# Performance work log

Measured on AMD Instinct MI355X. Metric: run time of the kernel, lower is better.

The kernel has to match this reference:

```python
import jax, jax.numpy as jnp
import numpy as np

ALPHA = 0.2  # LeakyReLU negative slope


def setup_inputs() -> dict:
    key = jax.random.key(0)
    k1, k2, k3, k4 = jax.random.split(key, 4)
    bs, n, fin = 8, 1024, 256
    heads, fo = 8, 64
    h = jax.random.normal(k1, (bs, n, fin), dtype=jnp.float32)
    adj = jax.random.randint(k2, (bs, n, n), 0, 2, dtype=jnp.int32)
    # W stored as [in_features, heads*out] so Wh = h @ W (same math as torch Linear)
    W = jax.random.normal(k3, (fin, heads * fo), dtype=jnp.float32) * 0.1
    a = jax.random.normal(k4, (heads, 2 * fo), dtype=jnp.float32) * 0.1
    return {"h": h, "adj": adj, "W": W, "a": a}


def reference(h, adj, W, a):
    bs, n, _ = h.shape
    heads, two_fo = a.shape
    fo = two_fo // 2
    # Wh: [bs, n, heads, fo]
    Wh = (h @ W).reshape(bs, n, heads, fo)
    a_src, a_dst = a[:, :fo], a[:, fo:]
    # Additive attention decomposed: e[b,h,i,j] = leaky_relu(src[b,h,i] + dst[b,h,j])
    e_src = jnp.einsum('bnhf,hf->bhn', Wh, a_src)  # [bs, heads, n]
    e_dst = jnp.einsum('bnhf,hf->bhn', Wh, a_dst)
    e = e_src[:, :, :, None] + e_dst[:, :, None, :]  # [bs, heads, n, n]
    e = jnp.where(e > 0, e, ALPHA * e)  # LeakyReLU
    e = jnp.where(adj[:, None, :, :] == 0, -jnp.inf, e)
    attn = jax.nn.softmax(e, axis=-1)  # [bs, heads, n, n]
    # h_prime[b,i,h,f] = sum_j attn[b,h,i,j] * Wh[b,j,h,f]
    h_prime = jnp.einsum('bhij,bjhf->bihf', attn, Wh)
    return h_prime.reshape(bs, n, heads * fo)
```

## Files before the change

kernel.cpp:

```cpp
#include <hip/hip_runtime.h>
#include <hip/hip_bf16.h>
#include <math.h>

#define BS 8
#define NN 1024
#define FIN 256
#define HEADS 8
#define FO 64
#define NH (HEADS*FO)
static constexpr float ALPHA = 0.2f;
static constexpr float LOG2E = 1.4426950408889634f;

typedef short bf16x8 __attribute__((ext_vector_type(8)));
typedef float f32x4  __attribute__((ext_vector_type(4)));
typedef unsigned short u16;
typedef unsigned u32;
typedef u16 u16x4v __attribute__((ext_vector_type(4)));
typedef u16 u16x8v __attribute__((ext_vector_type(8)));

__device__ __forceinline__ u16 f2b(float x) {
    __hip_bfloat16 b = __float2bfloat16(x);
    return *reinterpret_cast<u16*>(&b);
}
__device__ __forceinline__ float fexp2(float x) {
#if __has_builtin(__builtin_amdgcn_exp2f)
    return __builtin_amdgcn_exp2f(x);
#else
    float r; asm("v_exp_f32 %0, %1" : "=v"(r) : "v"(x)); return r;
#endif
}
__device__ __forceinline__ void gload_lds16(const void* g, void* l) {
    __builtin_amdgcn_global_load_lds(
        (const __attribute__((address_space(1))) unsigned int*)g,
        (__attribute__((address_space(3))) unsigned int*)l, 16, 0, 0);
}

__global__ __launch_bounds__(256) void prep_misc(const float* __restrict__ h,
                                                 const int* __restrict__ adj,
                                                 const float* __restrict__ W,
                                                 u16* __restrict__ hb,
                                                 u16* __restrict__ WbT,
                                                 u32* __restrict__ bits) {
    const int bid = blockIdx.x;
    const int t = threadIdx.x;
    if (bid < 8192) {
        const int lane = t & 63;
        const size_t e0 = ((size_t)bid * 256 + t) * 4;
        const int4 v = *reinterpret_cast<const int4*>(adj + e0);
        u32 x = (v.x ? 1u : 0u) | (v.y ? 2u : 0u) | (v.z ? 4u : 0u) | (v.w ? 8u : 0u);
        {   const u32 r = (u32)__shfl_xor((int)x, 1);
            const int sh = (lane & 1) * 4;  x = (x << sh) | (r << (4 - sh)); }
        {   const u32 r = (u32)__shfl_xor((int)x, 2);
            const int sh = (lane & 2) * 4;  x = (x << sh) | (r << (8 - sh)); }
        {   const u32 r = (u32)__shfl_xor((int)x, 4);
            const int sh = (lane & 4) * 4;  x = (x << sh) | (r << (16 - sh)); }
        if ((lane & 7) == 0) bits[e0 >> 5] = x;
    } else if (bid < 9216) {
        const int i = ((bid - 8192) * 256 + t) * 8;
        const float4 v0 = *reinterpret_cast<const float4*>(h + i);
        const float4 v1 = *reinterpret_cast<const float4*>(h + i + 4);
        u16x8v o;
        o[0]=f2b(v0.x); o[1]=f2b(v0.y); o[2]=f2b(v0.z); o[3]=f2b(v0.w);
        o[4]=f2b(v1.x); o[5]=f2b(v1.y); o[6]=f2b(v1.z); o[7]=f2b(v1.w);
        *reinterpret_cast<u16x8v*>(hb + i) = o;
    } else {
        __shared__ float T[64][65];
        const int bb = bid - 9216;
        const int hh = bb & 7;
        const int n0 = hh * 64, k0 = (bb >> 3) * 64;
        const int r4 = t >> 6, c = t & 63;
        #pragma unroll
        for (int p = 0; p < 16; ++p) {
            const int r = p * 4 + r4;
            T[r][c] = W[(size_t)(k0 + r) * NH + n0 + c];
        }
        __syncthreads();
        #pragma unroll
        for (int p = 0; p < 16; ++p) {
            const int r = p * 4 + r4;
            WbT[(size_t)(n0 + r) * FIN + k0 + c] = f2b(T[c][r]);
        }
    }
}

__global__ __launch_bounds__(256) void gemm_whT(const u16* __restrict__ hb,
                                                const u16* __restrict__ WbT,
                                                const float* __restrict__ avec,
                                                u16* __restrict__ WhT,
                                                float* __restrict__ esrc,
                                                float* __restrict__ edst) {
    __shared__ u16 Al[2][64 * 64];
    __shared__ u16 Bl[2][64 * 64];
    const int t = threadIdx.x, wv = t >> 6, lane = t & 63;
    const int g = lane >> 4, l15 = lane & 15;
    const int lid = (blockIdx.x & 7) * 128 + (blockIdx.x >> 3);
    const int m0 = (lid >> 3) * 64;
    const int h  = lid & 7;
    const int lr = lane >> 3;
    const int sch = (lane & 7) ^ lr;
    const int bh = (m0 >> 10) * HEADS + h;

    f32x4 acc[4] = {};

    auto stageA = [&](int buf, int k0) {
        #pragma unroll
        for (int c = 0; c < 2; ++c) {
            const int rowb = wv * 16 + c * 8;
            gload_lds16(hb + (size_t)(m0 + rowb + lr) * FIN + k0 + sch * 8,
                        &Al[buf][rowb * 64]);
        }
    };
    auto stageB = [&](int buf, int k0) {
        #pragma unroll
        for (int c = 0; c < 2; ++c) {
            const int rowb = wv * 16 + c * 8;
            gload_lds16(WbT + (size_t)(h * 64 + rowb + lr) * FIN + k0 + sch * 8,
                        &Bl[buf][rowb * 64]);
        }
    };

    stageA(0, 0); stageB(0, 0);
    __syncthreads();
    for (int kt = 0; kt < 4; ++kt) {
        const int buf = kt & 1;
        if (kt < 3) { stageA(buf ^ 1, (kt + 1) * 64); stageB(buf ^ 1, (kt + 1) * 64); }
        #pragma unroll
        for (int ks = 0; ks < 2; ++ks) {
            const int ch = (ks * 4 + g) ^ (l15 & 7);
            const bf16x8 afr = *reinterpret_cast<const bf16x8*>(
                &Al[buf][(wv * 16 + l15) * 64 + ch * 8]);
            #pragma unroll
            for (int n = 0; n < 4; ++n) {
                const bf16x8 bfr = *reinterpret_cast<const bf16x8*>(
                    &Bl[buf][(n * 16 + l15) * 64 + ch * 8]);
                acc[n] = __builtin_amdgcn_mfma_f32_16x16x32_bf16(afr, bfr, acc[n], 0, 0, 0);
            }
        }
        __syncthreads();
    }

    {
        float as_[4], ad_[4];
        #pragma unroll
        for (int n = 0; n < 4; ++n) {
            as_[n] = avec[h * 128 + n * 16 + l15] * LOG2E;
            ad_[n] = avec[h * 128 + 64 + n * 16 + l15] * LOG2E;
        }
        #pragma unroll
        for (int r = 0; r < 4; ++r) {
            float ps = acc[0][r] * as_[0] + acc[1][r] * as_[1]
                     + acc[2][r] * as_[2] + acc[3][r] * as_[3];
            float pd = acc[0][r] * ad_[0] + acc[1][r] * ad_[1]
                     + acc[2][r] * ad_[2] + acc[3][r] * ad_[3];
            #pragma unroll
            for (int off = 1; off < 16; off <<= 1) {
                ps += __shfl_xor(ps, off);
                pd += __shfl_xor(pd, off);
            }
            if (l15 == 0) {
                const int i = (m0 + wv * 16 + g * 4 + r) & (NN - 1);
                esrc[(size_t)bh * NN + i] = ps;
                edst[(size_t)bh * NN + i] = pd;
            }
        }
    }

    u16* scr = &Al[0][0];
    #pragma unroll
    for (int n = 0; n < 4; ++n) {
        u16x4v pk;
        #pragma unroll
        for (int r = 0; r < 4; ++r) pk[r] = f2b(acc[n][r]);
        *reinterpret_cast<u16x4v*>(&scr[(n * 16 + l15) * 72 + wv * 16 + g * 4]) = pk;
    }
    __syncthreads();
    const int il0 = m0 & (NN - 1);
    const int f = t >> 2, q = t & 3;
    const u16x8v v0 = *reinterpret_cast<const u16x8v*>(&scr[f * 72 + q * 16]);
    const u16x8v v1 = *reinterpret_cast<const u16x8v*>(&scr[f * 72 + q * 16 + 8]);
    u16* dst = &WhT[((size_t)bh * 64 + f) * NN + il0 + q * 16];
    *reinterpret_cast<u16x8v*>(dst)     = v0;
    *reinterpret_cast<u16x8v*>(dst + 8) = v1;
}

__global__ __launch_bounds__(128, 4) void attn_pv(const u32* __restrict__ bits,
                                                  const u16* __restrict__ WhT,
                                                  const float* __restrict__ esrc,
                                                  const float* __restrict__ edst,
                                                  float* __restrict__ out) {
    __shared__ u16 Bs[2][64 * 64];
    const int t = threadIdx.x, wv = t >> 6, lane = t & 63;
    const int g = lane >> 4, l15 = lane & 15;
    const int lr = lane >> 3, sch = (lane & 7) ^ lr;

    const int lid = (blockIdx.x & 7) * 256 + (blockIdx.x >> 3);
    const int it = lid & 31, h = (lid >> 5) & 7, b = lid >> 8;
    const int i0 = it * 32;
    const int bh = b * HEADS + h;
    const int rowi = i0 + wv * 16 + l15;

    const float es = esrc[(size_t)bh * NN + rowi];
    const u16*  whb = WhT + (size_t)bh * 64 * NN;
    const float* ed = edst + (size_t)bh * NN + 8 * g;
    const u32*  bitrow = bits + (size_t)(b * NN + rowi) * 32;

    auto stageB = [&](int buf, int j0) {
        #pragma unroll
        for (int c = 0; c < 4; ++c) {
            const int fb = wv * 32 + c * 8;
            gload_lds16(whb + (size_t)(fb + lr) * NN + j0 + sch * 8,
                        &Bs[buf][fb * 64]);
        }
    };

    stageB(0, 0);
    float4 peA[2], peB[2];
    u32    pwS[2];
    #pragma unroll
    for (int s = 0; s < 2; ++s) {
        peA[s] = *(const float4*)(ed + s * 32);
        peB[s] = *(const float4*)(ed + s * 32 + 4);
        pwS[s] = bitrow[s];
    }
    __syncthreads();

    f32x4 acc[4] = {};
    f32x4 dsum = {};
    bf16x8 ones;
    #pragma unroll
    for (int q = 0; q < 8; ++q) ones[q] = (short)0x3F80;

    for (int tt = 0; tt < 16; ++tt) {
        const int buf = tt & 1;
        const bool more = (tt < 15);
        if (more) {
            stageB(buf ^ 1, (tt + 1) * 64);
            asm volatile("" ::: "memory");
        }
        #pragma unroll
        for (int ks = 0; ks < 2; ++ks) {
            const int s = tt * 2 + ks;
            const float4 e0 = peA[ks], e1 = peB[ks];
            const u32 word = pwS[ks];
            if (more) {
                peA[ks] = *(const float4*)(ed + (s + 2) * 32);
                peB[ks] = *(const float4*)(ed + (s + 2) * 32 + 4);
                pwS[ks] = bitrow[s + 2];
            }
            const int chb = ((ks * 4 + g) ^ (l15 & 7)) * 8;
            const bf16x8 v0 = *(const bf16x8*)(&Bs[buf][(0 * 16 + l15) * 64 + chb]);
            const bf16x8 v1 = *(const bf16x8*)(&Bs[buf][(1 * 16 + l15) * 64 + chb]);
            const bf16x8 v2 = *(const bf16x8*)(&Bs[buf][(2 * 16 + l15) * 64 + chb]);
            const bf16x8 v3 = *(const bf16x8*)(&Bs[buf][(3 * 16 + l15) * 64 + chb]);

            const u32 byte_ = (word >> (8 * g)) & 0xffu;
            float ps[8];
            {
                float sv;
                sv = es + e0.x; sv = fmaxf(sv, ALPHA * sv); sv = (byte_ & 1u)        ? sv : -1e30f; ps[0] = fexp2(sv);
                sv = es + e0.y; sv = fmaxf(sv, ALPHA * sv); sv = ((byte_ >> 1) & 1u) ? sv : -1e30f; ps[1] = fexp2(sv);
                sv = es + e0.z; sv = fmaxf(sv, ALPHA * sv); sv = ((byte_ >> 2) & 1u) ? sv : -1e30f; ps[2] = fexp2(sv);
                sv = es + e0.w; sv = fmaxf(sv, ALPHA * sv); sv = ((byte_ >> 3) & 1u) ? sv : -1e30f; ps[3] = fexp2(sv);
                sv = es + e1.x; sv = fmaxf(sv, ALPHA * sv); sv = ((byte_ >> 4) & 1u) ? sv : -1e30f; ps[4] = fexp2(sv);
                sv = es + e1.y; sv = fmaxf(sv, ALPHA * sv); sv = ((byte_ >> 5) & 1u) ? sv : -1e30f; ps[5] = fexp2(sv);
                sv = es + e1.z; sv = fmaxf(sv, ALPHA * sv); sv = ((byte_ >> 6) & 1u) ? sv : -1e30f; ps[6] = fexp2(sv);
                sv = es + e1.w; sv = fmaxf(sv, ALPHA * sv); sv = ((byte_ >> 7) & 1u) ? sv : -1e30f; ps[7] = fexp2(sv);
            }
            union { u32 u[4]; bf16x8 v; } af;
            #pragma unroll
            for (int qp = 0; qp < 4; ++qp) {
                union { __hip_bfloat162 b2; u32 w; } cv;
                cv.b2 = __float22bfloat162_rn(make_float2(ps[2*qp], ps[2*qp+1]));
                af.u[qp] = cv.w;
            }
            __builtin_amdgcn_s_setprio(1);
            acc[0] = __builtin_amdgcn_mfma_f32_16x16x32_bf16(af.v, v0, acc[0], 0, 0, 0);
            acc[1] = __builtin_amdgcn_mfma_f32_16x16x32_bf16(af.v, v1, acc[1], 0, 0, 0);
            acc[2] = __builtin_amdgcn_mfma_f32_16x16x32_bf16(af.v, v2, acc[2], 0, 0, 0);
            acc[3] = __builtin_amdgcn_mfma_f32_16x16x32_bf16(af.v, v3, acc[3], 0, 0, 0);
            dsum   = __builtin_amdgcn_mfma_f32_16x16x32_bf16(af.v, ones, dsum, 0, 0, 0);
            __builtin_amdgcn_s_setprio(0);
        }
        if (more) {
            asm volatile("s_waitcnt vmcnt(6)" ::: "memory");
            __builtin_amdgcn_s_barrier();
        }
    }

    float inv[4];
    #pragma unroll
    for (int r = 0; r < 4; ++r) inv[r] = 1.0f / dsum[r];
    #pragma unroll
    for (int n = 0; n < 4; ++n)
        #pragma unroll
        for (int r = 0; r < 4; ++r) {
            const int io = i0 + wv * 16 + g * 4 + r;
            out[(size_t)(b * NN + io) * NH + h * 64 + n * 16 + l15] =
                acc[n][r] * inv[r];
        }
}

extern "C" void kernel_launch(void* const* d_in, const int* in_sizes, int n_in,
                              void* d_out, int out_size, void* d_ws, size_t ws_size,
                              hipStream_t stream) {
    const float* h   = (const float*)d_in[0];
    const int*   adj = (const int*)  d_in[1];
    const float* W   = (const float*)d_in[2];
    const float* a   = (const float*)d_in[3];
    float* out = (float*)d_out;

    char* p = (char*)d_ws;
    u16*   hb   = (u16*)p;   p += (size_t)BS * NN * FIN * 2;
    u16*   WbT  = (u16*)p;   p += (size_t)NH * FIN * 2;
    u16*   WhT  = (u16*)p;   p += (size_t)BS * HEADS * FO * NN * 2;
    float* esrc = (float*)p; p += (size_t)BS * HEADS * NN * 4;
    float* edst = (float*)p; p += (size_t)BS * HEADS * NN * 4;
    u32*   bits = (u32*)p;

    prep_misc<<<9248, 256, 0, stream>>>(h, adj, W, hb, WbT, bits);
    gemm_whT <<<1024, 256, 0, stream>>>(hb, WbT, a, WhT, esrc, edst);
    attn_pv  <<<2048, 128, 0, stream>>>(bits, WhT, esrc, edst, out);
}
```

Baseline: 51.35 us.

## Split attention K-loop across wave pairs with LDS reduction and 64-row tiles

Reorganizes attn_pv into 512-thread blocks that each cover 64 query rows. Four row-waves are each paired with a second wave that handles the other 32-column half of every 64-column K tile, and the partial accumulators and denominators are reduced through shared memory at the end. This doubles the reuse of each staged WhT tile across query rows and spreads the global-to-LDS staging over eight waves, one load per thread. In exchange it adds an LDS combine step, an extra barrier, and larger blocks that may limit occupancy.

```diff
diff --git a/kernel.cpp b/kernel.cpp
--- a/kernel.cpp
+++ b/kernel.cpp
@@ -183,46 +183,41 @@
     *reinterpret_cast<u16x8v*>(dst + 8) = v1;
 }
 
-__global__ __launch_bounds__(128, 4) void attn_pv(const u32* __restrict__ bits,
+__global__ __launch_bounds__(512, 8) void attn_pv(const u32* __restrict__ bits,
                                                   const u16* __restrict__ WhT,
                                                   const float* __restrict__ esrc,
                                                   const float* __restrict__ edst,
                                                   float* __restrict__ out) {
     __shared__ u16 Bs[2][64 * 64];
+    __shared__ float Cmb[4][64][21];
     const int t = threadIdx.x, wv = t >> 6, lane = t & 63;
     const int g = lane >> 4, l15 = lane & 15;
     const int lr = lane >> 3, sch = (lane & 7) ^ lr;
-
-    const int lid = (blockIdx.x & 7) * 256 + (blockIdx.x >> 3);
-    const int it = lid & 31, h = (lid >> 5) & 7, b = lid >> 8;
-    const int i0 = it * 32;
+    const int ks = wv >> 2;
+    const int wr = wv & 3;
+
+    const int lid = (blockIdx.x & 7) * 128 + (blockIdx.x >> 3);
+    const int it = lid & 15, h = (lid >> 4) & 7, b = lid >> 7;
+    const int i0 = it * 64;
     const int bh = b * HEADS + h;
-    const int rowi = i0 + wv * 16 + l15;
-
-    const float es = esrc[(size_t)bh * NN + rowi];
+    const int row0 = i0 + wr * 16 + l15;
+
+    const float es = esrc[(size_t)bh * NN + row0];
     const u16*  whb = WhT + (size_t)bh * 64 * NN;
-    const float* ed = edst + (size_t)bh * NN + 8 * g;
-    const u32*  bitrow = bits + (size_t)(b * NN + rowi) * 32;
-
-    auto stageB = [&](int buf, int j0) {
-        #pragma unroll
-        for (int c = 0; c < 4; ++c) {
-            const int fb = wv * 32 + c * 8;
-            gload_lds16(whb + (size_t)(fb + lr) * NN + j0 + sch * 8,
-                        &Bs[buf][fb * 64]);
-        }
+    const float* ed = edst + (size_t)bh * NN + ks * 32 + 8 * g;
+    const u32*  bitrow = bits + (size_t)(b * NN + row0) * 32 + ks;
+
+    auto stage = [&](int buf, int j0) {
+        gload_lds16(whb + (size_t)(wv * 8 + lr) * NN + j0 + sch * 8,
+                    &Bs[buf][wv * 8 * 64]);
     };
 
-    stageB(0, 0);
-    float4 peA[2], peB[2];
-    u32    pwS[2];
-    #pragma unroll
-    for (int s = 0; s < 2; ++s) {
-        peA[s] = *(const float4*)(ed + s * 32);
-        peB[s] = *(const float4*)(ed + s * 32 + 4);
-        pwS[s] = bitrow[s];
-    }
-    __syncthreads();
+    stage(0, 0);
+    float4 peA = *(const float4*)(ed);
+    float4 peB = *(const float4*)(ed + 4);
+    u32    pw  = bitrow[0];
+    asm volatile("s_waitcnt vmcnt(3)" ::: "memory");
+    __builtin_amdgcn_s_barrier();
 
     f32x4 acc[4] = {};
     f32x4 dsum = {};
@@ -230,74 +225,83 @@
     #pragma unroll
     for (int q = 0; q < 8; ++q) ones[q] = (short)0x3F80;
 
+    const int bsB = l15 * 128 + (((ks * 4 + g) ^ (l15 & 7)) << 4);
+
     for (int tt = 0; tt < 16; ++tt) {
         const int buf = tt & 1;
         const bool more = (tt < 15);
+        const float4 e0 = peA, e1 = peB;
+        const u32 word = pw;
         if (more) {
-            stageB(buf ^ 1, (tt + 1) * 64);
+            stage(buf ^ 1, (tt + 1) * 64);
             asm volatile("" ::: "memory");
-        }
-        #pragma unroll
-        for (int ks = 0; ks < 2; ++ks) {
-            const int s = tt * 2 + ks;
-            const float4 e0 = peA[ks], e1 = peB[ks];
-            const u32 word = pwS[ks];
-            if (more) {
-                peA[ks] = *(const float4*)(ed + (s + 2) * 32);
-                peB[ks] = *(const float4*)(ed + (s + 2) * 32 + 4);
-                pwS[ks] = bitrow[s + 2];
+            peA = *(const float4*)(ed + (tt + 1) * 64);
+            peB = *(const float4*)(ed + (tt + 1) * 64 + 4);
+            pw  = bitrow[(tt + 1) * 2];
+        }
+        const char* bsb = (const char*)&Bs[buf][0] + bsB;
+        const bf16x8 v0 = *(const bf16x8*)(bsb);
+        const bf16x8 v1 = *(const bf16x8*)(bsb + 2048);
+        const bf16x8 v2 = *(const bf16x8*)(bsb + 4096);
+        const bf16x8 v3 = *(const bf16x8*)(bsb + 6144);
+
+        const u32 byte_ = (word >> (8 * g)) & 0xffu;
+        float ps[8];
+        {
+            float sv;
+            sv = es + e0.x; sv = fmaxf(sv, ALPHA * sv); sv = (byte_ & 1u)        ? sv : -1e30f; ps[0] = fexp2(sv);
+            sv = es + e0.y; sv = fmaxf(sv, ALPHA * sv); sv = ((byte_ >> 1) & 1u) ? sv : -1e30f; ps[1] = fexp2(sv);
+            sv = es + e0.z; sv = fmaxf(sv, ALPHA * sv); sv = ((byte_ >> 2) & 1u) ? sv : -1e30f; ps[2] = fexp2(sv);
+            sv = es + e0.w; sv = fmaxf(sv, ALPHA * sv); sv = ((byte_ >> 3) & 1u) ? sv : -1e30f; ps[3] = fexp2(sv);
+            sv = es + e1.x; sv = fmaxf(sv, ALPHA * sv); sv = ((byte_ >> 4) & 1u) ? sv : -1e30f; ps[4] = fexp2(sv);
+            sv = es + e1.y; sv = fmaxf(sv, ALPHA * sv); sv = ((byte_ >> 5) & 1u) ? sv : -1e30f; ps[5] = fexp2(sv);
+            sv = es + e1.z; sv = fmaxf(sv, ALPHA * sv); sv = ((byte_ >> 6) & 1u) ? sv : -1e30f; ps[6] = fexp2(sv);
+            sv = es + e1.w; sv = fmaxf(sv, ALPHA * sv); sv = ((byte_ >> 7) & 1u) ? sv : -1e30f; ps[7] = fexp2(sv);
+        }
+        union { u32 u[4]; bf16x8 v; } af;
+        #pragma unroll
+        for (int qp = 0; qp < 4; ++qp) {
+            union { __hip_bfloat162 b2; u32 w; } cv;
+            cv.b2 = __float22bfloat162_rn(make_float2(ps[2*qp], ps[2*qp+1]));
+            af.u[qp] = cv.w;
+        }
+        __builtin_amdgcn_s_setprio(1);
+        acc[0] = __builtin_amdgcn_mfma_f32_16x16x32_bf16(af.v, v0, acc[0], 0, 0, 0);
+        acc[1] = __builtin_amdgcn_mfma_f32_16x16x32_bf16(af.v, v1, acc[1], 0, 0, 0);
+        acc[2] = __builtin_amdgcn_mfma_f32_16x16x32_bf16(af.v, v2, acc[2], 0, 0, 0);
+        acc[3] = __builtin_amdgcn_mfma_f32_16x16x32_bf16(af.v, v3, acc[3], 0, 0, 0);
+        dsum   = __builtin_amdgcn_mfma_f32_16x16x32_bf16(af.v, ones, dsum, 0, 0, 0);
+        __builtin_amdgcn_s_setprio(0);
+        if (more) {
+            asm volatile("s_waitcnt vmcnt(3)" ::: "memory");
+            __builtin_amdgcn_s_barrier();
+        }
+    }
+
+    if (ks) {
+        float* cm = &Cmb[wr][lane][0];
+        #pragma unroll
+        for (int n = 0; n < 4; ++n)
+            #pragma unroll
+            for (int r = 0; r < 4; ++r) cm[n * 4 + r] = acc[n][r];
+        #pragma unroll
+        for (int r = 0; r < 4; ++r) cm[16 + r] = dsum[r];
+    }
+    __syncthreads();
+    if (!ks) {
+        const float* cm = &Cmb[wr][lane][0];
+        float inv[4];
+        #pragma unroll
+        for (int r = 0; r < 4; ++r) inv[r] = 1.0f / (dsum[r] + cm[16 + r]);
+        #pragma unroll
+        for (int n = 0; n < 4; ++n)
+            #pragma unroll
+            for (int r = 0; r < 4; ++r) {
+                const int io = i0 + wr * 16 + g * 4 + r;
+                out[(size_t)(b * NN + io) * NH + h * 64 + n * 16 + l15] =
+                    (acc[n][r] + cm[n * 4 + r]) * inv[r];
             }
-            const int chb = ((ks * 4 + g) ^ (l15 & 7)) * 8;
-            const bf16x8 v0 = *(const bf16x8*)(&Bs[buf][(0 * 16 + l15) * 64 + chb]);
-            const bf16x8 v1 = *(const bf16x8*)(&Bs[buf][(1 * 16 + l15) * 64 + chb]);
-            const bf16x8 v2 = *(const bf16x8*)(&Bs[buf][(2 * 16 + l15) * 64 + chb]);
-            const bf16x8 v3 = *(const bf16x8*)(&Bs[buf][(3 * 16 + l15) * 64 + chb]);
-
-            const u32 byte_ = (word >> (8 * g)) & 0xffu;
-            float ps[8];
-            {
-                float sv;
-                sv = es + e0.x; sv = fmaxf(sv, ALPHA * sv); sv = (byte_ & 1u)        ? sv : -1e30f; ps[0] = fexp2(sv);
-                sv = es + e0.y; sv = fmaxf(sv, ALPHA * sv); sv = ((byte_ >> 1) & 1u) ? sv : -1e30f; ps[1] = fexp2(sv);
-                sv = es + e0.z; sv = fmaxf(sv, ALPHA * sv); sv = ((byte_ >> 2) & 1u) ? sv : -1e30f; ps[2] = fexp2(sv);
-                sv = es + e0.w; sv = fmaxf(sv, ALPHA * sv); sv = ((byte_ >> 3) & 1u) ? sv : -1e30f; ps[3] = fexp2(sv);
-                sv = es + e1.x; sv = fmaxf(sv, ALPHA * sv); sv = ((byte_ >> 4) & 1u) ? sv : -1e30f; ps[4] = fexp2(sv);
-                sv = es + e1.y; sv = fmaxf(sv, ALPHA * sv); sv = ((byte_ >> 5) & 1u) ? sv : -1e30f; ps[5] = fexp2(sv);
-                sv = es + e1.z; sv = fmaxf(sv, ALPHA * sv); sv = ((byte_ >> 6) & 1u) ? sv : -1e30f; ps[6] = fexp2(sv);
-                sv = es + e1.w; sv = fmaxf(sv, ALPHA * sv); sv = ((byte_ >> 7) & 1u) ? sv : -1e30f; ps[7] = fexp2(sv);
-            }
-            union { u32 u[4]; bf16x8 v; } af;
-            #pragma unroll
-            for (int qp = 0; qp < 4; ++qp) {
-                union { __hip_bfloat162 b2; u32 w; } cv;
-                cv.b2 = __float22bfloat162_rn(make_float2(ps[2*qp], ps[2*qp+1]));
-                af.u[qp] = cv.w;
-            }
-            __builtin_amdgcn_s_setprio(1);
-            acc[0] = __builtin_amdgcn_mfma_f32_16x16x32_bf16(af.v, v0, acc[0], 0, 0, 0);
-            acc[1] = __builtin_amdgcn_mfma_f32_16x16x32_bf16(af.v, v1, acc[1], 0, 0, 0);
-            acc[2] = __builtin_amdgcn_mfma_f32_16x16x32_bf16(af.v, v2, acc[2], 0, 0, 0);
-            acc[3] = __builtin_amdgcn_mfma_f32_16x16x32_bf16(af.v, v3, acc[3], 0, 0, 0);
-            dsum   = __builtin_amdgcn_mfma_f32_16x16x32_bf16(af.v, ones, dsum, 0, 0, 0);
-            __builtin_amdgcn_s_setprio(0);
-        }
-        if (more) {
-            asm volatile("s_waitcnt vmcnt(6)" ::: "memory");
-            __builtin_amdgcn_s_barrier();
-        }
-    }
-
-    float inv[4];
-    #pragma unroll
-    for (int r = 0; r < 4; ++r) inv[r] = 1.0f / dsum[r];
-    #pragma unroll
-    for (int n = 0; n < 4; ++n)
-        #pragma unroll
-        for (int r = 0; r < 4; ++r) {
-            const int io = i0 + wv * 16 + g * 4 + r;
-            out[(size_t)(b * NN + io) * NH + h * 64 + n * 16 + l15] =
-                acc[n][r] * inv[r];
-        }
+    }
 }
 
 extern "C" void kernel_launch(void* const* d_in, const int* in_sizes, int n_in,
@@ -319,5 +323,5 @@
 
     prep_misc<<<9248, 256, 0, stream>>>(h, adj, W, hb, WbT, bits);
     gemm_whT <<<1024, 256, 0, stream>>>(hb, WbT, a, WhT, esrc, edst);
-    attn_pv  <<<2048, 128, 0, stream>>>(bits, WhT, esrc, edst, out);
-}
+    attn_pv  <<<1024, 512, 0, stream>>>(bits, WhT, esrc, edst, out);
+}
```

New measurement: 69.65 us. 35.6% more time.
